# Performance work log

Measured on AMD Instinct MI355X. Metric: run time of the kernel, lower is better.

## Reference

```python
import jax, jax.numpy as jnp
import numpy as np

N = 1_000_000          # number of fusion candidate pairs
H, W = 200, 70400      # sparse buffer dims hard-coded in the module
FILL = -9999999.0


def _init_conv(k, co, ci):
    # torch Conv2d default init: U(-1/sqrt(fan_in), 1/sqrt(fan_in)), 1x1 kernel
    bound = 1.0 / np.sqrt(ci)
    kw, kb = jax.random.split(k)
    w = jax.random.uniform(kw, (co, ci), jnp.float32, -bound, bound)
    b = jax.random.uniform(kb, (co,), jnp.float32, -bound, bound)
    return w, b


def setup_inputs() -> dict:
    key = jax.random.key(0)
    ks = jax.random.split(key, 7)
    input_1 = jax.random.normal(ks[0], (1, 4, 1, N), dtype=jnp.float32)
    idx0 = jax.random.randint(ks[1], (N,), 0, H)   # row in [0,200)
    idx1 = jax.random.randint(ks[2], (N,), 0, W)   # col in [0,70400)
    tensor_index = jnp.stack([idx0, idx1], axis=1).astype(jnp.int64)
    w1, b1 = _init_conv(ks[3], 18, 4)
    w2, b2 = _init_conv(ks[4], 36, 18)
    w3, b3 = _init_conv(ks[5], 36, 36)
    w4, b4 = _init_conv(ks[6], 1, 36)
    return dict(input_1=input_1, tensor_index=tensor_index,
                w1=w1, b1=b1, w2=w2, b2=b2, w3=w3, b3=b3, w4=w4, b4=b4)


def _fuse_2d_3d(x, w1, b1, w2, b2, w3, b3, w4, b4):
    # x: (4, N); 1x1 convs over a (1,C,1,N) tensor == per-point channel matmuls
    h = jax.nn.relu(w1 @ x + b1[:, None])
    h = jax.nn.relu(w2 @ h + b2[:, None])
    h = jax.nn.relu(w3 @ h + b3[:, None])
    return w4 @ h + b4[:, None]  # (1, N)


def reference(input_1, tensor_index, w1, b1, w2, b2, w3, b3, w4, b4):
    base = jnp.full((1, H, W), FILL, dtype=input_1.dtype)

    def scatter_branch(_):
        feat = _fuse_2d_3d(input_1[0, :, 0, :], w1, b1, w2, b2, w3, b3, w4, b4)  # (1, N)
        out = base.at[:, tensor_index[:, 0], tensor_index[:, 1]].set(feat)
        return out, jnp.int32(1)

    def empty_branch(_):
        return base, jnp.int32(0)

    out_1, flag = jax.lax.cond(tensor_index[0, 0] == -1,
                               empty_branch, scatter_branch, None)
    # MaxPool2d([200,1]) over (C=1,H=200,W) -> max over H; squeeze+reshape -> (1, W, 1)
    x = jnp.max(out_1, axis=1)            # (1, W)
    return x.reshape(1, -1, 1), flag
```

## Files before the change

### kernel.cpp

```cpp
#include <hip/hip_runtime.h>

#define N_PTS 1000000
#define H_DIM 200
#define W_DIM 70400
#define FILL_V -9999999.0f

__global__ void __launch_bounds__(256, 2) mlp_scatter_kernel(
    const float* __restrict__ input,
    const int* __restrict__ tindex,
    const float* __restrict__ w1, const float* __restrict__ b1,
    const float* __restrict__ w2, const float* __restrict__ b2,
    const float* __restrict__ w3, const float* __restrict__ b3,
    const float* __restrict__ w4, const float* __restrict__ b4,
    int* __restrict__ counts,
    uint2* __restrict__ list,
    int maxk)
{
    __shared__ float4 sw1[18];
    __shared__ float4 sw2[36 * 5];
    __shared__ float4 sw3[36 * 9];
    __shared__ float4 sw4[9];
    __shared__ float  sb1[18], sb2[36], sb3[36];
    __shared__ float  sb4;

    const int t = threadIdx.x;
    {
        float* p = (float*)sw1;
        for (int k = t; k < 72; k += 256) p[k] = w1[k];
        p = (float*)sw2;
        for (int k = t; k < 720; k += 256) {
            int r = k / 20, c = k % 20;
            p[k] = (c < 18) ? w2[r * 18 + c] : 0.0f;
        }
        p = (float*)sw3;
        for (int k = t; k < 1296; k += 256) p[k] = w3[k];
        p = (float*)sw4;
        for (int k = t; k < 36; k += 256) p[k] = w4[k];
        for (int k = t; k < 18; k += 256) sb1[k] = b1[k];
        for (int k = t; k < 36; k += 256) sb2[k] = b2[k];
        for (int k = t; k < 36; k += 256) sb3[k] = b3[k];
        if (t == 0) sb4 = b4[0];
    }
    __syncthreads();

    if (tindex[0] == -1) return;

    const int i = blockIdx.x * 256 + t;
    if (i >= N_PTS) return;

    const float x0 = input[0 * N_PTS + i];
    const float x1 = input[1 * N_PTS + i];
    const float x2 = input[2 * N_PTS + i];
    const float x3 = input[3 * N_PTS + i];

    float h1[20];
#pragma unroll
    for (int o = 0; o < 18; ++o) {
        const float4 wv = sw1[o];
        float a = sb1[o];
        a = fmaf(wv.x, x0, a); a = fmaf(wv.y, x1, a);
        a = fmaf(wv.z, x2, a); a = fmaf(wv.w, x3, a);
        h1[o] = fmaxf(a, 0.0f);
    }
    h1[18] = 0.0f; h1[19] = 0.0f;

    float h2[36];
#pragma unroll
    for (int o = 0; o < 36; ++o) {
        float a = sb2[o];
#pragma unroll
        for (int q = 0; q < 5; ++q) {
            const float4 wv = sw2[o * 5 + q];
            a = fmaf(wv.x, h1[q * 4 + 0], a);
            a = fmaf(wv.y, h1[q * 4 + 1], a);
            a = fmaf(wv.z, h1[q * 4 + 2], a);
            a = fmaf(wv.w, h1[q * 4 + 3], a);
        }
        h2[o] = fmaxf(a, 0.0f);
    }

    float h3[36];
#pragma unroll
    for (int o = 0; o < 36; ++o) {
        float a = sb3[o];
#pragma unroll
        for (int q = 0; q < 9; ++q) {
            const float4 wv = sw3[o * 9 + q];
            a = fmaf(wv.x, h2[q * 4 + 0], a);
            a = fmaf(wv.y, h2[q * 4 + 1], a);
            a = fmaf(wv.z, h2[q * 4 + 2], a);
            a = fmaf(wv.w, h2[q * 4 + 3], a);
        }
        h3[o] = fmaxf(a, 0.0f);
    }

    float v = sb4;
#pragma unroll
    for (int q = 0; q < 9; ++q) {
        const float4 wv = sw4[q];
        v = fmaf(wv.x, h3[q * 4 + 0], v);
        v = fmaf(wv.y, h3[q * 4 + 1], v);
        v = fmaf(wv.z, h3[q * 4 + 2], v);
        v = fmaf(wv.w, h3[q * 4 + 3], v);
    }

    const int2 hw = ((const int2*)tindex)[i];
    const int pos = atomicAdd(&counts[hw.y], 1);
    if (pos < maxk) {
        uint2 e;
        e.x = __float_as_uint(v);
        e.y = ((unsigned)i << 8) | (unsigned)hw.x;
        list[(size_t)hw.y * maxk + pos] = e;
    }
}

__global__ void __launch_bounds__(256) colmax_kernel(
    const int* __restrict__ tindex,
    const int* __restrict__ counts,
    const uint2* __restrict__ list,
    float* __restrict__ out,
    int maxk)
{
    __shared__ unsigned long long rowwin[4][200];
    const int lane = threadIdx.x;
    const int y    = threadIdx.y;
    const int w    = blockIdx.x * 4 + y;

    const bool empty = (tindex[0] == -1);

    if (blockIdx.x == 0 && lane == 0 && y == 0)
        out[W_DIM] = empty ? 0.0f : 1.0f;

    int c = 0;
    if (!empty) {
        c = counts[w];
        if (c > maxk) c = maxk;
    }

    unsigned long long* tbl = rowwin[y];
    tbl[lane]       = 0ull;
    tbl[lane + 64]  = 0ull;
    tbl[lane + 128] = 0ull;
    if (lane < 8) tbl[lane + 192] = 0ull;
    __syncthreads();

    uint2 e = make_uint2(0u, 0u);
    const bool have = (lane < c);
    if (have) {
        e = list[(size_t)w * maxk + lane];
        const unsigned long long key64 =
            ((unsigned long long)e.y << 32) | (unsigned long long)e.x;
        atomicMax(&tbl[e.y & 0xFFu], key64);
    }
    __syncthreads();

    float v = FILL_V;
    if (have) {
        const unsigned long long winner = tbl[e.y & 0xFFu];
        v = __uint_as_float((unsigned)(winner & 0xFFFFFFFFull));
    }
#pragma unroll
    for (int off = 32; off > 0; off >>= 1)
        v = fmaxf(v, __shfl_down(v, off, 64));

    if (lane == 0) out[w] = v;
}

extern "C" void kernel_launch(void* const* d_in, const int* in_sizes, int n_in,
                              void* d_out, int out_size, void* d_ws, size_t ws_size,
                              hipStream_t stream) {
    const float* input  = (const float*)d_in[0];
    const int*   tindex = (const int*)d_in[1];
    const float* w1 = (const float*)d_in[2];
    const float* b1 = (const float*)d_in[3];
    const float* w2 = (const float*)d_in[4];
    const float* b2 = (const float*)d_in[5];
    const float* w3 = (const float*)d_in[6];
    const float* b3 = (const float*)d_in[7];
    const float* w4 = (const float*)d_in[8];
    const float* b4 = (const float*)d_in[9];
    float* out = (float*)d_out;

    int*   counts = (int*)d_ws;
    uint2* list   = (uint2*)((char*)d_ws + (size_t)W_DIM * sizeof(int));

    size_t avail = (ws_size > (size_t)W_DIM * sizeof(int))
                       ? ws_size - (size_t)W_DIM * sizeof(int) : 0;
    int maxk = (int)(avail / ((size_t)W_DIM * sizeof(uint2)));
    if (maxk > 64) maxk = 64;
    if (maxk < 1)  maxk = 1;

    hipMemsetAsync(counts, 0, (size_t)W_DIM * sizeof(int), stream);

    mlp_scatter_kernel<<<(N_PTS + 255) / 256, 256, 0, stream>>>(
        input, tindex, w1, b1, w2, b2, w3, b3, w4, b4, counts, list, maxk);

    colmax_kernel<<<W_DIM / 4, dim3(64, 4), 0, stream>>>(
        tindex, counts, list, out, maxk);
}
```

Baseline: 199.2 us.

## Read MLP weights directly via uniform global loads instead of LDS staging

Removes the per-block staging of all MLP weights into shared memory and the barrier that follows it. The weights are now indexed straight from global memory with wave-uniform addresses, which the compiler can turn into scalar loads served from the scalar cache. The last layer is folded into the third layer's loop so the h3 array is no longer kept, and the two-waves-per-SIMD occupancy hint is dropped. In exchange the kernel issues many more scalar loads, which may stall or raise register pressure.

```diff
diff --git a/kernel.cpp b/kernel.cpp
--- a/kernel.cpp
+++ b/kernel.cpp
@@ -5,7 +5,7 @@
 #define W_DIM 70400
 #define FILL_V -9999999.0f
 
-__global__ void __launch_bounds__(256, 2) mlp_scatter_kernel(
+__global__ void __launch_bounds__(256) mlp_scatter_kernel(
     const float* __restrict__ input,
     const int* __restrict__ tindex,
     const float* __restrict__ w1, const float* __restrict__ b1,
@@ -16,36 +16,9 @@
     uint2* __restrict__ list,
     int maxk)
 {
-    __shared__ float4 sw1[18];
-    __shared__ float4 sw2[36 * 5];
-    __shared__ float4 sw3[36 * 9];
-    __shared__ float4 sw4[9];
-    __shared__ float  sb1[18], sb2[36], sb3[36];
-    __shared__ float  sb4;
-
-    const int t = threadIdx.x;
-    {
-        float* p = (float*)sw1;
-        for (int k = t; k < 72; k += 256) p[k] = w1[k];
-        p = (float*)sw2;
-        for (int k = t; k < 720; k += 256) {
-            int r = k / 20, c = k % 20;
-            p[k] = (c < 18) ? w2[r * 18 + c] : 0.0f;
-        }
-        p = (float*)sw3;
-        for (int k = t; k < 1296; k += 256) p[k] = w3[k];
-        p = (float*)sw4;
-        for (int k = t; k < 36; k += 256) p[k] = w4[k];
-        for (int k = t; k < 18; k += 256) sb1[k] = b1[k];
-        for (int k = t; k < 36; k += 256) sb2[k] = b2[k];
-        for (int k = t; k < 36; k += 256) sb3[k] = b3[k];
-        if (t == 0) sb4 = b4[0];
-    }
-    __syncthreads();
-
     if (tindex[0] == -1) return;
 
-    const int i = blockIdx.x * 256 + t;
+    const int i = blockIdx.x * 256 + threadIdx.x;
     if (i >= N_PTS) return;
 
     const float x0 = input[0 * N_PTS + i];
@@ -53,55 +26,35 @@
     const float x2 = input[2 * N_PTS + i];
     const float x3 = input[3 * N_PTS + i];
 
-    float h1[20];
+    float h1[18];
 #pragma unroll
     for (int o = 0; o < 18; ++o) {
-        const float4 wv = sw1[o];
-        float a = sb1[o];
-        a = fmaf(wv.x, x0, a); a = fmaf(wv.y, x1, a);
-        a = fmaf(wv.z, x2, a); a = fmaf(wv.w, x3, a);
+        float a = b1[o];
+        a = fmaf(w1[o * 4 + 0], x0, a);
+        a = fmaf(w1[o * 4 + 1], x1, a);
+        a = fmaf(w1[o * 4 + 2], x2, a);
+        a = fmaf(w1[o * 4 + 3], x3, a);
         h1[o] = fmaxf(a, 0.0f);
     }
-    h1[18] = 0.0f; h1[19] = 0.0f;
 
     float h2[36];
 #pragma unroll
     for (int o = 0; o < 36; ++o) {
-        float a = sb2[o];
+        float a = b2[o];
 #pragma unroll
-        for (int q = 0; q < 5; ++q) {
-            const float4 wv = sw2[o * 5 + q];
-            a = fmaf(wv.x, h1[q * 4 + 0], a);
-            a = fmaf(wv.y, h1[q * 4 + 1], a);
-            a = fmaf(wv.z, h1[q * 4 + 2], a);
-            a = fmaf(wv.w, h1[q * 4 + 3], a);
-        }
+        for (int k = 0; k < 18; ++k)
+            a = fmaf(w2[o * 18 + k], h1[k], a);
         h2[o] = fmaxf(a, 0.0f);
     }
 
-    float h3[36];
+    float v = b4[0];
 #pragma unroll
     for (int o = 0; o < 36; ++o) {
-        float a = sb3[o];
+        float a = b3[o];
 #pragma unroll
-        for (int q = 0; q < 9; ++q) {
-            const float4 wv = sw3[o * 9 + q];
-            a = fmaf(wv.x, h2[q * 4 + 0], a);
-            a = fmaf(wv.y, h2[q * 4 + 1], a);
-            a = fmaf(wv.z, h2[q * 4 + 2], a);
-            a = fmaf(wv.w, h2[q * 4 + 3], a);
-        }
-        h3[o] = fmaxf(a, 0.0f);
-    }
-
-    float v = sb4;
-#pragma unroll
-    for (int q = 0; q < 9; ++q) {
-        const float4 wv = sw4[q];
-        v = fmaf(wv.x, h3[q * 4 + 0], v);
-        v = fmaf(wv.y, h3[q * 4 + 1], v);
-        v = fmaf(wv.z, h3[q * 4 + 2], v);
-        v = fmaf(wv.w, h3[q * 4 + 3], v);
+        for (int k = 0; k < 36; ++k)
+            a = fmaf(w3[o * 36 + k], h2[k], a);
+        v = fmaf(w4[o], fmaxf(a, 0.0f), v);
     }
 
     const int2 hw = ((const int2*)tindex)[i];
```

Measured after the change: 192.7 us. 3.3% less time.
